# Optimization experiments

Hardware: AMD Instinct MI355X
Metric: run time of the kernel (lower is better)

## Reference

```python
import jax, jax.numpy as jnp
import numpy as np
import math

HIDDEN = 1024
N_HEADS = 16
HEAD_DIM = HIDDEN // N_HEADS  # 64
B, S = 4, 8192


def setup_inputs() -> dict:
    key = jax.random.key(0)
    ks = jax.random.split(key, 5)
    scale = 1.0 / math.sqrt(HIDDEN)
    return {
        "hidden_states": jax.random.normal(ks[0], (B, S, HIDDEN), dtype=jnp.float32),
        "Wq": jax.random.normal(ks[1], (HIDDEN, HIDDEN), dtype=jnp.float32) * scale,
        "Wk": jax.random.normal(ks[2], (HIDDEN, HIDDEN), dtype=jnp.float32) * scale,
        "Wv": jax.random.normal(ks[3], (HIDDEN, HIDDEN), dtype=jnp.float32) * scale,
        "Wo": jax.random.normal(ks[4], (HIDDEN, HIDDEN), dtype=jnp.float32) * scale,
    }


def reference(hidden_states, Wq, Wk, Wv, Wo):
    b, s, _ = hidden_states.shape
    # nn.Linear(bias=False): y = x @ W.T
    q = (hidden_states @ Wq.T).reshape(b, s, N_HEADS, HEAD_DIM)
    k = (hidden_states @ Wk.T).reshape(b, s, N_HEADS, HEAD_DIM)
    v = (hidden_states @ Wv.T).reshape(b, s, N_HEADS, HEAD_DIM)
    # Faithful to source: NO transpose to (b,h,s,d); matmul contracts head_dim
    # per (batch, position), yielding [b, s, h, h] head-mixing weights.
    attn = jnp.einsum("bshd,bstd->bsht", q, k) / math.sqrt(HEAD_DIM)
    attn = jax.nn.softmax(attn, axis=-1)
    out = jnp.einsum("bsht,bstd->bshd", attn, v).reshape(b, s, HIDDEN)
    return out @ Wo.T
```

## Files before the change

### kernel.cpp

```cpp
#include <hip/hip_runtime.h>
#include <hip/hip_bf16.h>


typedef short bf16x8 __attribute__((ext_vector_type(8)));
typedef float f32x4  __attribute__((ext_vector_type(4)));

__device__ __forceinline__ float bf2f(short u) {
    union { unsigned int ui; float f; } cv;
    cv.ui = ((unsigned int)(unsigned short)u) << 16;
    return cv.f;
}
__device__ __forceinline__ short f2bf(float f) {
    __hip_bfloat16 h = __float2bfloat16(f);
    return *reinterpret_cast<short*>(&h);
}

__device__ __forceinline__ void gload_lds16(const void* g, void* lds) {
    const unsigned __attribute__((address_space(1)))* gp =
        reinterpret_cast<const unsigned __attribute__((address_space(1)))*>((unsigned long long)g);
    unsigned __attribute__((address_space(3)))* lp =
        reinterpret_cast<unsigned __attribute__((address_space(3)))*>(
            (unsigned int)(unsigned long long)lds);
    __builtin_amdgcn_global_load_lds(gp, lp, 16, 0, 0);
}

__global__ void detect_dtype(const unsigned* __restrict__ x, int* __restrict__ flag) {
    __shared__ int cnt;
    if (threadIdx.x == 0) cnt = 0;
    __syncthreads();
    int c = 0;
    for (int i = threadIdx.x; i < 4096; i += 256) {
        const unsigned u = x[(long)i * 4001 + 3];
        const unsigned b = (u >> 7) & 0xFF;
        c += (b >= 0x70 && b <= 0x87) ? 1 : 0;
    }
    atomicAdd(&cnt, c);
    __syncthreads();
    if (threadIdx.x == 0) *flag = (cnt > 2048) ? 0 : 1;
}

__global__ void convert_any(const void* __restrict__ src, long eoff,
                            short* __restrict__ dst, long n,
                            const int* __restrict__ flag) {
    const int f = *flag;
    const long step = (long)gridDim.x * blockDim.x * 8;
    for (long i = ((long)blockIdx.x * blockDim.x + threadIdx.x) * 8; i < n; i += step) {
        if (f) {
            const float* s = (const float*)src + eoff + i;
            const f32x4 a = *(const f32x4*)s;
            const f32x4 b = *(const f32x4*)(s + 4);
            bf16x8 o;
            o[0] = f2bf(a[0]); o[1] = f2bf(a[1]); o[2] = f2bf(a[2]); o[3] = f2bf(a[3]);
            o[4] = f2bf(b[0]); o[5] = f2bf(b[1]); o[6] = f2bf(b[2]); o[7] = f2bf(b[3]);
            *(bf16x8*)(dst + i) = o;
        } else {
            *(bf16x8*)(dst + i) = *(const bf16x8*)((const short*)src + eoff + i);
        }
    }
}

__device__ __forceinline__ void gemm256_core(const short* __restrict__ A,
                                             const short* __restrict__ W,
                                             void* __restrict__ C,
                                             const int* flag_fp32,
                                             long m0, int n0, short* lds) {
    constexpr int K = 1024, N = 1024;
    const int tid  = threadIdx.x;
    const int lane = tid & 63;
    const int wid  = tid >> 6;
    const int wm = wid >> 2, wn = wid & 3;

    short* A0 = lds;
    short* B0 = lds + 16384;
    short* A1 = lds + 32768;
    short* B1 = lds + 49152;

    const int srl = tid >> 3;
    const int kcs = (tid & 7) ^ (srl & 7);
    int aoff[4], boff[4];
    #pragma unroll
    for (int i = 0; i < 4; ++i) {
        const int row = i * 64 + srl;
        aoff[i] = (int)((m0 + row) * K + kcs * 8);
        boff[i] = (n0 + row) * K + kcs * 8;
    }
    const int ldsw = wid * 512;

    f32x4 acc[8][4] = {};

    #pragma unroll
    for (int i = 0; i < 4; ++i) gload_lds16(A + aoff[i], A0 + i * 4096 + ldsw);
    #pragma unroll
    for (int i = 0; i < 4; ++i) gload_lds16(W + boff[i], B0 + i * 4096 + ldsw);
    asm volatile("s_waitcnt vmcnt(0)" ::: "memory");
    __builtin_amdgcn_s_barrier();
    __builtin_amdgcn_sched_barrier(0);

    const int arow = wm * 128 + (lane & 15);
    const int brow = wn * 64 + (lane & 15);
    const int kx0 = (((lane >> 4)) ^ (lane & 7)) * 8;
    const int kx1 = ((4 + (lane >> 4)) ^ (lane & 7)) * 8;

    for (int t = 0; t < 16; ++t) {
        const int cur = t & 1;
        const short* rA = cur ? A1 : A0;
        const short* rB = cur ? B1 : B0;
        short* sA = cur ? A0 : A1;
        short* sB = cur ? B0 : B1;
        const int kadd = (t + 1) * 64;
        const bool more = (t < 15);

        bf16x8 af0[8], bf0[4], af1[8], bf1[4];
        #pragma unroll
        for (int m = 0; m < 8; ++m)
            af0[m] = *(const bf16x8*)(rA + (arow + m * 16) * 64 + kx0);
        #pragma unroll
        for (int n = 0; n < 4; ++n)
            bf0[n] = *(const bf16x8*)(rB + (brow + n * 16) * 64 + kx0);
        if (more) {
            #pragma unroll
            for (int i = 0; i < 4; ++i)
                gload_lds16(A + aoff[i] + kadd, sA + i * 4096 + ldsw);
            #pragma unroll
            for (int i = 0; i < 4; ++i)
                gload_lds16(W + boff[i] + kadd, sB + i * 4096 + ldsw);
        }
        __builtin_amdgcn_s_setprio(1);
        #pragma unroll
        for (int m = 0; m < 8; ++m) {
            af1[m] = *(const bf16x8*)(rA + (arow + m * 16) * 64 + kx1);
            if (m >= 4)
                bf1[m - 4] = *(const bf16x8*)(rB + (brow + (m - 4) * 16) * 64 + kx1);
            #pragma unroll
            for (int n = 0; n < 4; ++n)
                acc[m][n] = __builtin_amdgcn_mfma_f32_16x16x32_bf16(
                                af0[m], bf0[n], acc[m][n], 0, 0, 0);
        }
        #pragma unroll
        for (int m = 0; m < 8; ++m)
            #pragma unroll
            for (int n = 0; n < 4; ++n)
                acc[m][n] = __builtin_amdgcn_mfma_f32_16x16x32_bf16(
                                af1[m], bf1[n], acc[m][n], 0, 0, 0);
        __builtin_amdgcn_s_setprio(0);
        __builtin_amdgcn_sched_barrier(0);
        if (more) {
            asm volatile("s_waitcnt vmcnt(0)" ::: "memory");
            __builtin_amdgcn_s_barrier();
            __builtin_amdgcn_sched_barrier(0);
        }
    }

    const int f = flag_fp32 ? *flag_fp32 : 0;
    #pragma unroll
    for (int mf = 0; mf < 8; ++mf) {
        #pragma unroll
        for (int nf = 0; nf < 4; ++nf) {
            const int  col   = n0 + wn * 64 + nf * 16 + (lane & 15);
            const long rbase = m0 + wm * 128 + mf * 16 + (lane >> 4) * 4;
            if (f) {
                float* Cf = (float*)C;
                #pragma unroll
                for (int r = 0; r < 4; ++r)
                    Cf[(rbase + r) * N + col] = acc[mf][nf][r];
            } else {
                short* Cs = (short*)C;
                #pragma unroll
                for (int r = 0; r < 4; ++r)
                    Cs[(rbase + r) * N + col] = f2bf(acc[mf][nf][r]);
            }
        }
    }
}

__global__ __launch_bounds__(512, 2) void gemm_qkv256(const short* __restrict__ A,
                                                      const short* __restrict__ W0,
                                                      const short* __restrict__ W1,
                                                      const short* __restrict__ W2,
                                                      short* __restrict__ C0,
                                                      short* __restrict__ C1,
                                                      short* __restrict__ C2) {
    __shared__ __align__(16) short lds[65536];
    const int nwg = gridDim.x;
    const int q8  = nwg >> 3;
    const int d   = blockIdx.x;
    const int lin = (d & 7) * q8 + (d >> 3);
    const int x   = lin / 12;
    const int r   = lin - x * 12;
    const int yy  = r / 3;
    const int z   = r - yy * 3;
    const short* W = (z == 0) ? W0 : (z == 1) ? W1 : W2;
    short*       C = (z == 0) ? C0 : (z == 1) ? C1 : C2;
    gemm256_core(A, W, C, nullptr, (long)x * 256, yy * 256, lds);
}

__global__ __launch_bounds__(512, 2) void gemm_out256(const short* __restrict__ A,
                                                      const short* __restrict__ W,
                                                      void* __restrict__ C,
                                                      long moff,
                                                      const int* __restrict__ flag) {
    __shared__ __align__(16) short lds[65536];
    const int nwg = gridDim.x;
    const int q8  = nwg >> 3;
    const int d   = blockIdx.x;
    const int lin = (d & 7) * q8 + (d >> 3);
    const int x   = lin >> 2;
    const int yy  = lin & 3;
    gemm256_core(A, W, C, flag, moff + (long)x * 256, yy * 256, lds);
}

__global__ __launch_bounds__(256) void attn_mix(const short* __restrict__ Q,
                                                const short* __restrict__ K,
                                                const short* __restrict__ V,
                                                short* __restrict__ Z) {
    constexpr int RS = 72;
    __shared__ short sq[4][16 * RS];
    __shared__ short sk[4][16 * RS];
    __shared__ short sv[4][16 * RS];
    __shared__ float sp[4][256];

    const int  tid  = threadIdx.x;
    const int  lane = tid & 63;
    const int  w    = tid >> 6;
    const long tok  = (long)blockIdx.x * 4 + w;

    const short* qg = Q + tok * 1024;
    const short* kg = K + tok * 1024;
    const short* vg = V + tok * 1024;

    #pragma unroll
    for (int it = 0; it < 2; ++it) {
        const int c   = lane + 64 * it;
        const int row = c >> 3;
        const int cc  = (c & 7) * 8;
        *(bf16x8*)&sq[w][row * RS + cc] = *(const bf16x8*)(qg + c * 8);
        *(bf16x8*)&sk[w][row * RS + cc] = *(const bf16x8*)(kg + c * 8);
        *(bf16x8*)&sv[w][row * RS + cc] = *(const bf16x8*)(vg + c * 8);
    }
    __syncthreads();

    const int h  = lane >> 2;
    const int t0 = (lane & 3) * 4;
    float sc[4] = {0.f, 0.f, 0.f, 0.f};
    for (int d = 0; d < 64; ++d) {
        const float qv = bf2f(sq[w][h * RS + d]);
        #pragma unroll
        for (int j = 0; j < 4; ++j)
            sc[j] += qv * bf2f(sk[w][(t0 + j) * RS + d]);
    }
    #pragma unroll
    for (int j = 0; j < 4; ++j) sc[j] *= 0.125f;

    float mx = fmaxf(fmaxf(sc[0], sc[1]), fmaxf(sc[2], sc[3]));
    mx = fmaxf(mx, __shfl_xor(mx, 1));
    mx = fmaxf(mx, __shfl_xor(mx, 2));
    float ex[4], s = 0.f;
    #pragma unroll
    for (int j = 0; j < 4; ++j) { ex[j] = __expf(sc[j] - mx); s += ex[j]; }
    s += __shfl_xor(s, 1);
    s += __shfl_xor(s, 2);
    const float inv = 1.f / s;
    #pragma unroll
    for (int j = 0; j < 4; ++j) sp[w][h * 16 + t0 + j] = ex[j] * inv;
    __syncthreads();

    const int dbase = (lane & 3) * 16;
    float o[16] = {};
    for (int t = 0; t < 16; ++t) {
        const float p = sp[w][h * 16 + t];
        const bf16x8 v0 = *(const bf16x8*)&sv[w][t * RS + dbase];
        const bf16x8 v1 = *(const bf16x8*)&sv[w][t * RS + dbase + 8];
        #pragma unroll
        for (int e = 0; e < 8; ++e) {
            o[e]     += p * bf2f(v0[e]);
            o[e + 8] += p * bf2f(v1[e]);
        }
    }
    bf16x8 ov0, ov1;
    #pragma unroll
    for (int e = 0; e < 8; ++e) { ov0[e] = f2bf(o[e]); ov1[e] = f2bf(o[e + 8]); }
    *(bf16x8*)(Z + tok * 1024 + lane * 16)     = ov0;
    *(bf16x8*)(Z + tok * 1024 + lane * 16 + 8) = ov1;
}

extern "C" void kernel_launch(void* const* d_in, const int* in_sizes, int n_in,
                              void* d_out, int out_size, void* d_ws, size_t ws_size,
                              hipStream_t stream) {
    const void* X = d_in[0];

    const long TOT = 32768;
    constexpr long WELEM = 1024 * 1024;

    char* ws   = (char*)d_ws;
    int*  flag = (int*)ws;
    short* Wqb = (short*)(ws + 256);
    short* Wkb = Wqb + WELEM;
    short* Wvb = Wkb + WELEM;
    short* Wob = Wvb + WELEM;
    short* dyn = Wob + WELEM;

    const size_t fixed = 256 + 4 * WELEM * 2;
    long chunk = 256;
    const long tiers[4] = {32768, 8192, 2048, 512};
    for (int i = 0; i < 4; ++i)
        if (fixed + (size_t)6 * tiers[i] * 1024 * 2 <= ws_size) { chunk = tiers[i]; break; }

    short* Xb = dyn;
    short* Qb = Xb + chunk * 1024;
    short* Kb = Qb + chunk * 1024;
    short* Vb = Kb + chunk * 1024;
    short* Zb = Vb + chunk * 1024;

    detect_dtype<<<1, 256, 0, stream>>>((const unsigned*)X, flag);
    convert_any<<<512, 256, 0, stream>>>(d_in[1], 0, Wqb, WELEM, flag);
    convert_any<<<512, 256, 0, stream>>>(d_in[2], 0, Wkb, WELEM, flag);
    convert_any<<<512, 256, 0, stream>>>(d_in[3], 0, Wvb, WELEM, flag);
    convert_any<<<512, 256, 0, stream>>>(d_in[4], 0, Wob, WELEM, flag);

    for (long t0 = 0; t0 < TOT; t0 += chunk) {
        convert_any<<<2048, 256, 0, stream>>>(X, t0 * 1024, Xb, chunk * 1024, flag);
        gemm_qkv256<<<dim3((chunk / 256) * 12), 512, 0, stream>>>(Xb, Wqb, Wkb, Wvb,
                                                                  Qb, Kb, Vb);
        attn_mix<<<dim3(chunk / 4), 256, 0, stream>>>(Qb, Kb, Vb, Zb);
        gemm_out256<<<dim3((chunk / 256) * 4), 512, 0, stream>>>(Zb - t0 * 1024, Wob,
                                                                 d_out, t0, flag);
    }
}
```

Measured before the change: 427.8 us.

## Deepen GEMM LDS prefetch to two tiles ahead with partial vmcnt waits

The GEMM main loop now preloads the first two K-tiles into the two LDS buffers. Each later tile load is issued right after the compute that consumed that buffer, so data is fetched two iterations ahead. Each iteration waits with vmcnt(8) rather than draining all loads, so only the current tile has to have landed. The aim is to hide more global-to-LDS latency behind the MFMA work, at the cost of a second block barrier per iteration.

```diff
diff --git a/kernel.cpp b/kernel.cpp
--- a/kernel.cpp
+++ b/kernel.cpp
@@ -70,10 +70,8 @@
     const int wid  = tid >> 6;
     const int wm = wid >> 2, wn = wid & 3;
 
-    short* A0 = lds;
-    short* B0 = lds + 16384;
-    short* A1 = lds + 32768;
-    short* B1 = lds + 49152;
+    short* Abuf[2] = { lds,         lds + 32768 };
+    short* Bbuf[2] = { lds + 16384, lds + 49152 };
 
     const int srl = tid >> 3;
     const int kcs = (tid & 7) ^ (srl & 7);
@@ -89,12 +87,13 @@
     f32x4 acc[8][4] = {};
 
     #pragma unroll
-    for (int i = 0; i < 4; ++i) gload_lds16(A + aoff[i], A0 + i * 4096 + ldsw);
-    #pragma unroll
-    for (int i = 0; i < 4; ++i) gload_lds16(W + boff[i], B0 + i * 4096 + ldsw);
-    asm volatile("s_waitcnt vmcnt(0)" ::: "memory");
-    __builtin_amdgcn_s_barrier();
-    __builtin_amdgcn_sched_barrier(0);
+    for (int i = 0; i < 4; ++i) gload_lds16(A + aoff[i], Abuf[0] + i * 4096 + ldsw);
+    #pragma unroll
+    for (int i = 0; i < 4; ++i) gload_lds16(W + boff[i], Bbuf[0] + i * 4096 + ldsw);
+    #pragma unroll
+    for (int i = 0; i < 4; ++i) gload_lds16(A + aoff[i] + 64, Abuf[1] + i * 4096 + ldsw);
+    #pragma unroll
+    for (int i = 0; i < 4; ++i) gload_lds16(W + boff[i] + 64, Bbuf[1] + i * 4096 + ldsw);
 
     const int arow = wm * 128 + (lane & 15);
     const int brow = wn * 64 + (lane & 15);
@@ -103,12 +102,16 @@
 
     for (int t = 0; t < 16; ++t) {
         const int cur = t & 1;
-        const short* rA = cur ? A1 : A0;
-        const short* rB = cur ? B1 : B0;
-        short* sA = cur ? A0 : A1;
-        short* sB = cur ? B0 : B1;
-        const int kadd = (t + 1) * 64;
-        const bool more = (t < 15);
+        const short* rA = Abuf[cur];
+        const short* rB = Bbuf[cur];
+        short* sA = Abuf[cur];
+        short* sB = Bbuf[cur];
+        const int kadd = (t + 2) * 64;
+
+        if (t < 15) asm volatile("s_waitcnt vmcnt(8)" ::: "memory");
+        else        asm volatile("s_waitcnt vmcnt(0)" ::: "memory");
+        __builtin_amdgcn_s_barrier();
+        __builtin_amdgcn_sched_barrier(0);
 
         bf16x8 af0[8], bf0[4], af1[8], bf1[4];
         #pragma unroll
@@ -117,14 +120,6 @@
         #pragma unroll
         for (int n = 0; n < 4; ++n)
             bf0[n] = *(const bf16x8*)(rB + (brow + n * 16) * 64 + kx0);
-        if (more) {
-            #pragma unroll
-            for (int i = 0; i < 4; ++i)
-                gload_lds16(A + aoff[i] + kadd, sA + i * 4096 + ldsw);
-            #pragma unroll
-            for (int i = 0; i < 4; ++i)
-                gload_lds16(W + boff[i] + kadd, sB + i * 4096 + ldsw);
-        }
         __builtin_amdgcn_s_setprio(1);
         #pragma unroll
         for (int m = 0; m < 8; ++m) {
@@ -144,10 +139,17 @@
                                 af1[m], bf1[n], acc[m][n], 0, 0, 0);
         __builtin_amdgcn_s_setprio(0);
         __builtin_amdgcn_sched_barrier(0);
-        if (more) {
-            asm volatile("s_waitcnt vmcnt(0)" ::: "memory");
+        if (t < 15) {
             __builtin_amdgcn_s_barrier();
             __builtin_amdgcn_sched_barrier(0);
+            if (t < 14) {
+                #pragma unroll
+                for (int i = 0; i < 4; ++i)
+                    gload_lds16(A + aoff[i] + kadd, sA + i * 4096 + ldsw);
+                #pragma unroll
+                for (int i = 0; i < 4; ++i)
+                    gload_lds16(W + boff[i] + kadd, sB + i * 4096 + ldsw);
+            }
         }
     }
 
```

After: 501.4 us. +17.2%, slower.

## Keep two K-tiles in flight with partial vmcnt waits in GEMM loop

Applied to the files above, without the earlier changes.

Restructures the GEMM main loop so both LDS buffers are filled up front and each buffer is refilled right after its compute finishes. Waits use vmcnt(8), so the next tile's loads stay outstanding while the current tile is consumed. This is meant to hide global-to-LDS latency better than the previous wait-for-all at every step. It adds extra barriers per iteration and exposes the first loads without overlap.

```diff
diff --git a/kernel.cpp b/kernel.cpp
--- a/kernel.cpp
+++ b/kernel.cpp
@@ -88,28 +88,22 @@
 
     f32x4 acc[8][4] = {};
 
-    #pragma unroll
-    for (int i = 0; i < 4; ++i) gload_lds16(A + aoff[i], A0 + i * 4096 + ldsw);
-    #pragma unroll
-    for (int i = 0; i < 4; ++i) gload_lds16(W + boff[i], B0 + i * 4096 + ldsw);
-    asm volatile("s_waitcnt vmcnt(0)" ::: "memory");
-    __builtin_amdgcn_s_barrier();
-    __builtin_amdgcn_sched_barrier(0);
-
     const int arow = wm * 128 + (lane & 15);
     const int brow = wn * 64 + (lane & 15);
     const int kx0 = (((lane >> 4)) ^ (lane & 7)) * 8;
     const int kx1 = ((4 + (lane >> 4)) ^ (lane & 7)) * 8;
 
-    for (int t = 0; t < 16; ++t) {
-        const int cur = t & 1;
-        const short* rA = cur ? A1 : A0;
-        const short* rB = cur ? B1 : B0;
-        short* sA = cur ? A0 : A1;
-        short* sB = cur ? B0 : B1;
-        const int kadd = (t + 1) * 64;
-        const bool more = (t < 15);
-
+    auto STAGE = [&](short* sA, short* sB, int t) {
+        const int kadd = t * 64;
+        #pragma unroll
+        for (int i = 0; i < 4; ++i)
+            gload_lds16(A + aoff[i] + kadd, sA + i * 4096 + ldsw);
+        #pragma unroll
+        for (int i = 0; i < 4; ++i)
+            gload_lds16(W + boff[i] + kadd, sB + i * 4096 + ldsw);
+    };
+
+    auto COMPUTE = [&](const short* rA, const short* rB) {
         bf16x8 af0[8], bf0[4], af1[8], bf1[4];
         #pragma unroll
         for (int m = 0; m < 8; ++m)
@@ -117,14 +111,6 @@
         #pragma unroll
         for (int n = 0; n < 4; ++n)
             bf0[n] = *(const bf16x8*)(rB + (brow + n * 16) * 64 + kx0);
-        if (more) {
-            #pragma unroll
-            for (int i = 0; i < 4; ++i)
-                gload_lds16(A + aoff[i] + kadd, sA + i * 4096 + ldsw);
-            #pragma unroll
-            for (int i = 0; i < 4; ++i)
-                gload_lds16(W + boff[i] + kadd, sB + i * 4096 + ldsw);
-        }
         __builtin_amdgcn_s_setprio(1);
         #pragma unroll
         for (int m = 0; m < 8; ++m) {
@@ -143,11 +129,29 @@
                 acc[m][n] = __builtin_amdgcn_mfma_f32_16x16x32_bf16(
                                 af1[m], bf1[n], acc[m][n], 0, 0, 0);
         __builtin_amdgcn_s_setprio(0);
+    };
+
+    STAGE(A0, B0, 0);
+    STAGE(A1, B1, 1);
+
+    for (int tt = 0; tt < 8; ++tt) {
+        const int t = tt * 2;
+        asm volatile("s_waitcnt vmcnt(8)" ::: "memory");
+        __builtin_amdgcn_s_barrier();
         __builtin_amdgcn_sched_barrier(0);
-        if (more) {
-            asm volatile("s_waitcnt vmcnt(0)" ::: "memory");
+        COMPUTE(A0, B0);
+        __builtin_amdgcn_sched_barrier(0);
+        __builtin_amdgcn_s_barrier();
+        if (t + 2 < 16) STAGE(A0, B0, t + 2);
+        if (tt < 7) asm volatile("s_waitcnt vmcnt(8)" ::: "memory");
+        else        asm volatile("s_waitcnt vmcnt(0)" ::: "memory");
+        __builtin_amdgcn_s_barrier();
+        __builtin_amdgcn_sched_barrier(0);
+        COMPUTE(A1, B1);
+        __builtin_amdgcn_sched_barrier(0);
+        if (tt < 7) {
             __builtin_amdgcn_s_barrier();
-            __builtin_amdgcn_sched_barrier(0);
+            if (t + 3 < 16) STAGE(A1, B1, t + 3);
         }
     }
 
```

Result: no change. 432.2 us (+1.0%).
